# Optimization experiments

Measured on AMD Instinct MI355X. Metric: run time of the kernel, lower is better.

Reference implementation:

```python
import jax, jax.numpy as jnp
import numpy as np

N_NODES = 50000
N_EDGES = 600000
D_IN = 128
D_HID = 256
D_EMB = 128
D_OUT = 2


def sage_conv(x, src, dst, Wl, Wr, b):
    # PyG SAGEConv (aggr='mean'): out_i = W_l @ mean_{j in N(i)} x_j + b + W_r @ x_i
    # edge_index[0]=src (j, message source), edge_index[1]=dst (i, target)
    agg = jax.ops.segment_sum(x[src], dst, num_segments=N_NODES)          # [N, d_in]
    cnt = jax.ops.segment_sum(jnp.ones_like(dst, dtype=x.dtype), dst,
                              num_segments=N_NODES)                        # [N]
    mean = agg / jnp.maximum(cnt, 1.0)[:, None]
    return mean @ Wl + x @ Wr + b


def setup_inputs() -> dict:
    key = jax.random.key(0)
    ks = jax.random.split(key, 12)
    def glorot(k, i, o):
        s = jnp.sqrt(2.0 / (i + o)).astype(jnp.float32)
        return jax.random.normal(k, (i, o), dtype=jnp.float32) * s
    x = jax.random.normal(ks[0], (N_NODES, D_IN), dtype=jnp.float32)
    edge_index = jax.random.randint(ks[1], (2, N_EDGES), 0, N_NODES, dtype=jnp.int64)
    return {
        "x": x,
        "edge_index": edge_index,
        "Wl1": glorot(ks[2], D_IN, D_HID),  "Wr1": glorot(ks[3], D_IN, D_HID),
        "b1": jnp.zeros((D_HID,), jnp.float32),
        "Wl2": glorot(ks[4], D_HID, D_HID), "Wr2": glorot(ks[5], D_HID, D_HID),
        "b2": jnp.zeros((D_HID,), jnp.float32),
        "Wl3": glorot(ks[6], D_HID, D_EMB), "Wr3": glorot(ks[7], D_HID, D_EMB),
        "b3": jnp.zeros((D_EMB,), jnp.float32),
        "Wout": glorot(ks[8], D_EMB, D_OUT),
        "bout": jnp.zeros((D_OUT,), jnp.float32),
    }


def reference(x, edge_index, Wl1, Wr1, b1, Wl2, Wr2, b2, Wl3, Wr3, b3, Wout, bout):
    src, dst = edge_index[0], edge_index[1]
    h = jax.nn.relu(sage_conv(x, src, dst, Wl1, Wr1, b1))   # dropout_rate=0 -> identity
    h = jax.nn.relu(sage_conv(h, src, dst, Wl2, Wr2, b2))
    h = sage_conv(h, src, dst, Wl3, Wr3, b3)
    return h @ Wout + bout                                   # [N, D_OUT]
```

## Files before the change

### kernel.cpp

```cpp
#include <hip/hip_runtime.h>
#include <hip/hip_fp8.h>


constexpr int D_IN  = 128;
constexpr int D_HID = 256;

typedef __attribute__((ext_vector_type(8))) short short8x;
typedef __attribute__((ext_vector_type(4))) float f32x4;
typedef __attribute__((ext_vector_type(2))) float f32x2;

__device__ inline unsigned bf16_rne(float f) {
    unsigned u = __float_as_uint(f);
    return (u + 0x7fffu + ((u >> 16) & 1u)) >> 16;
}


__device__ inline void prep_wt_elem(const float* __restrict__ Wl,
                                    const float* __restrict__ Wr,
                                    int K1, int K2, int Nc, int i,
                                    short* __restrict__ WTh) {
    const int KE = K1 + K2;
    const int KSTEPS = KE / 32;
    int e = i & 7;
    int t = i >> 3;
    int l = t & 63;
    int t2 = t >> 6;
    int k32 = t2 % KSTEPS;
    int n16 = t2 / KSTEPS;
    int n = n16 * 16 + (l & 15);
    int k = k32 * 32 + (l >> 4) * 8 + e;
    float w = (k < K1) ? Wl[(size_t)k * Nc + n] : Wr[(size_t)(k - K1) * Nc + n];
    WTh[i] = (short)bf16_rne(w);
}

__global__ __launch_bounds__(256) void setup_kernel(
    const float* __restrict__ Wl1, const float* __restrict__ Wr1,
    short* __restrict__ wt1h,
    const float* __restrict__ Wl2, const float* __restrict__ Wr2,
    short* __restrict__ wt2h,
    const float* __restrict__ Wl3, const float* __restrict__ Wr3,
    const float* __restrict__ b3, const float* __restrict__ Wout,
    const float* __restrict__ bout, float* __restrict__ Wc, float* __restrict__ bc,
    const float* __restrict__ x, unsigned short* __restrict__ xb,
    const int* __restrict__ dst, int* __restrict__ cnt,
    int Nn, int E) {
    const int gtid = blockIdx.x * blockDim.x + threadIdx.x;
    const int gs = gridDim.x * blockDim.x;

    const int n8 = Nn * D_IN / 8;
    for (int i = gtid; i < n8; i += gs) {
        const float4* p = (const float4*)(x + (size_t)i * 8);
        float4 v0 = p[0], v1 = p[1];
        float f[8] = {v0.x, v0.y, v0.z, v0.w, v1.x, v1.y, v1.z, v1.w};
        unsigned h[8];
        #pragma unroll
        for (int j = 0; j < 8; ++j) h[j] = bf16_rne(f[j]);
        uint4 qh;
        qh.x = h[0] | (h[1] << 16); qh.y = h[2] | (h[3] << 16);
        qh.z = h[4] | (h[5] << 16); qh.w = h[6] | (h[7] << 16);
        *(uint4*)(xb + (size_t)i * 8) = qh;
    }

    for (int i = gtid; i < E; i += gs)
        atomicAdd(&cnt[dst[i]], 1);

    for (int i = gtid; i < 256 * 256; i += gs)
        prep_wt_elem(Wl1, Wr1, 128, 128, 256, i, wt1h);
    for (int i = gtid; i < 256 * 512; i += gs)
        prep_wt_elem(Wl2, Wr2, 256, 256, 256, i, wt2h);

    if (gtid < 1024 * 16) {
        int d = gtid >> 4, sl = gtid & 15;
        int hh = d >> 2, c = d & 3;
        const float* Ws = (c < 2) ? Wl3 : Wr3;
        int o = c & 1;
        float s = 0.f;
        #pragma unroll
        for (int e = 0; e < 8; ++e) {
            int k = sl * 8 + e;
            s += Ws[hh * 128 + k] * Wout[k * 2 + o];
        }
        #pragma unroll
        for (int mk = 8; mk >= 1; mk >>= 1) s += __shfl_xor(s, mk, 16);
        if (sl == 0) Wc[d] = s;
    }
    if (gtid >= 16384 && gtid < 16416) {
        int o = (gtid >> 4) & 1, sl = gtid & 15;
        float s = 0.f;
        #pragma unroll
        for (int e = 0; e < 8; ++e) {
            int k = sl * 8 + e;
            s += b3[k] * Wout[k * 2 + o];
        }
        #pragma unroll
        for (int mk = 8; mk >= 1; mk >>= 1) s += __shfl_xor(s, mk, 16);
        if (sl == 0) bc[o] = s + bout[o];
    }
}


__global__ __launch_bounds__(1024) void scan_local_kernel(
    const int* __restrict__ cnt, int* __restrict__ row_ptr,
    int* __restrict__ bsums, int Nn) {
    __shared__ int wsum[16];
    const int tid = threadIdx.x, lane = tid & 63, wid = tid >> 6;
    const int idx0 = blockIdx.x * 4096 + tid * 4;
    int v[4];
    #pragma unroll
    for (int j = 0; j < 4; ++j) {
        int idx = idx0 + j;
        v[j] = (idx < Nn) ? cnt[idx] : 0;
    }
    int s = v[0] + v[1] + v[2] + v[3];
    int xi = s;
    #pragma unroll
    for (int o = 1; o < 64; o <<= 1) {
        int t = __shfl_up(xi, o, 64);
        if (lane >= o) xi += t;
    }
    if (lane == 63) wsum[wid] = xi;
    __syncthreads();
    if (wid == 0) {
        int t = (lane < 16) ? wsum[lane] : 0;
        #pragma unroll
        for (int o = 1; o < 16; o <<= 1) {
            int u = __shfl_up(t, o, 64);
            if (lane >= o) t += u;
        }
        if (lane < 16) wsum[lane] = t;
    }
    __syncthreads();
    int off = (wid ? wsum[wid - 1] : 0) + xi - s;
    int run = off;
    #pragma unroll
    for (int j = 0; j < 4; ++j) {
        int idx = idx0 + j;
        if (idx <= Nn) row_ptr[idx] = run;
        run += v[j];
    }
    if (tid == 0) bsums[blockIdx.x] = wsum[15];
}

__global__ __launch_bounds__(1024) void scan_add_kernel(
    int* __restrict__ row_ptr, int* __restrict__ cursor,
    const int* __restrict__ bsums, int Nn) {
    __shared__ int sbase;
    const int b = blockIdx.x;
    if (threadIdx.x == 0) {
        int s = 0;
        for (int i = 0; i < b; ++i) s += bsums[i];
        sbase = s;
    }
    __syncthreads();
    const int base = sbase;
    const int idx0 = b * 4096 + threadIdx.x * 4;
    #pragma unroll
    for (int j = 0; j < 4; ++j) {
        int idx = idx0 + j;
        if (idx <= Nn) {
            int v = row_ptr[idx] + base;
            row_ptr[idx] = v;
            if (idx < Nn) cursor[idx] = v;
        }
    }
}

__global__ __launch_bounds__(256) void scatter_kernel(
    const int* __restrict__ src, const int* __restrict__ dst,
    int* __restrict__ cursor, int* __restrict__ esrc, int E) {
    int i0 = (blockIdx.x * blockDim.x + threadIdx.x) * 4;
    if (i0 >= E) return;
    int n = E - i0; if (n > 4) n = 4;
    int s[4], p[4];
    for (int j = 0; j < n; ++j) s[j] = src[i0 + j];
    for (int j = 0; j < n; ++j) p[j] = atomicAdd(&cursor[dst[i0 + j]], 1);
    for (int j = 0; j < n; ++j) esrc[p[j]] = s[j];
}


__device__ inline void addbf8(const uint4& q, float* a) {
    a[0] += __uint_as_float(q.x << 16); a[1] += __uint_as_float(q.x & 0xFFFF0000u);
    a[2] += __uint_as_float(q.y << 16); a[3] += __uint_as_float(q.y & 0xFFFF0000u);
    a[4] += __uint_as_float(q.z << 16); a[5] += __uint_as_float(q.z & 0xFFFF0000u);
    a[6] += __uint_as_float(q.w << 16); a[7] += __uint_as_float(q.w & 0xFFFF0000u);
}

__device__ inline void addf8w(unsigned u, float* a) {
    f32x2 lo = __builtin_amdgcn_cvt_pk_f32_fp8((int)u, false);
    f32x2 hi = __builtin_amdgcn_cvt_pk_f32_fp8((int)u, true);
    a[0] += lo.x; a[1] += lo.y; a[2] += hi.x; a[3] += hi.y;
}

__device__ inline void addf8x16(const uint4& q, float* a) {
    addf8w(q.x, a + 0); addf8w(q.y, a + 4); addf8w(q.z, a + 8); addf8w(q.w, a + 12);
}


template <int K1, int K2, int N, bool RELU, bool TU, bool F8G, bool F8OUT>
__global__ __launch_bounds__(256, 4) void fused_gemm_kernel(
    const void* __restrict__ gsrc, const unsigned short* __restrict__ self,
    const int* __restrict__ row_ptr, const int* __restrict__ esrc,
    const short8x* __restrict__ WTh, const float* __restrict__ bias,
    unsigned short* __restrict__ C, unsigned char* __restrict__ C8,
    const float* __restrict__ Wc, const float* __restrict__ bc,
    float* __restrict__ tuout, int M) {
    constexpr int KEFF = K1 + K2;
    constexpr int KS32 = KEFF / 32;
    constexpr int NC1 = K1 / 8;
    constexpr int NC2 = K2 / 8;
    __shared__ __attribute__((aligned(16))) unsigned short sA[32][KEFF];
    __shared__ float4 sRed[4][32];
    const int tid = threadIdx.x, lane = tid & 63, wid = tid >> 6;
    const int bm = blockIdx.x * 32;

    #pragma unroll
    for (int pass = 0; pass < 2; ++pass) {
        const int nl = pass * 16 + wid * 4 + (lane >> 4);
        const int node = bm + nl;
        const int sl = lane & 15;
        if constexpr (!F8G) {
            float a0[8] = {}, a1[8] = {}, a2[8] = {}, a3[8] = {};
            float inv = 1.0f;
            if (node < M) {
                int beg = row_ptr[node], end = row_ptr[node + 1];
                const unsigned short* xg = (const unsigned short*)gsrc;
                int e = beg;
                for (; e + 4 <= end; e += 4) {
                    int s0 = esrc[e], s1 = esrc[e + 1], s2 = esrc[e + 2], s3 = esrc[e + 3];
                    uint4 q0 = *(const uint4*)(xg + (size_t)s0 * K1 + sl * 8);
                    uint4 q1 = *(const uint4*)(xg + (size_t)s1 * K1 + sl * 8);
                    uint4 q2 = *(const uint4*)(xg + (size_t)s2 * K1 + sl * 8);
                    uint4 q3 = *(const uint4*)(xg + (size_t)s3 * K1 + sl * 8);
                    addbf8(q0, a0); addbf8(q1, a1); addbf8(q2, a2); addbf8(q3, a3);
                }
                for (; e < end; ++e) {
                    uint4 q0 = *(const uint4*)(xg + (size_t)esrc[e] * K1 + sl * 8);
                    addbf8(q0, a0);
                }
                inv = 1.0f / fmaxf((float)(end - beg), 1.0f);
            }
            unsigned h[8];
            #pragma unroll
            for (int i = 0; i < 8; ++i)
                h[i] = bf16_rne((a0[i] + a1[i] + a2[i] + a3[i]) * inv);
            uint4 qh;
            qh.x = h[0] | (h[1] << 16); qh.y = h[2] | (h[3] << 16);
            qh.z = h[4] | (h[5] << 16); qh.w = h[6] | (h[7] << 16);
            int p = (sl & 8) | ((sl & 7) ^ (nl & 7));
            *(uint4*)&sA[nl][p * 8] = qh;
        } else {
            float a0[16] = {}, a1[16] = {};
            float inv = 1.0f;
            if (node < M) {
                int beg = row_ptr[node], end = row_ptr[node + 1];
                const unsigned char* xg = (const unsigned char*)gsrc;
                int e = beg;
                for (; e + 4 <= end; e += 4) {
                    int s0 = esrc[e], s1 = esrc[e + 1], s2 = esrc[e + 2], s3 = esrc[e + 3];
                    uint4 q0 = *(const uint4*)(xg + (size_t)s0 * K1 + sl * 16);
                    uint4 q1 = *(const uint4*)(xg + (size_t)s1 * K1 + sl * 16);
                    uint4 q2 = *(const uint4*)(xg + (size_t)s2 * K1 + sl * 16);
                    uint4 q3 = *(const uint4*)(xg + (size_t)s3 * K1 + sl * 16);
                    addf8x16(q0, a0); addf8x16(q1, a1); addf8x16(q2, a0); addf8x16(q3, a1);
                }
                for (; e < end; ++e) {
                    uint4 q0 = *(const uint4*)(xg + (size_t)esrc[e] * K1 + sl * 16);
                    addf8x16(q0, a0);
                }
                inv = 1.0f / fmaxf((float)(end - beg), 1.0f);
            }
            unsigned h[16];
            #pragma unroll
            for (int i = 0; i < 16; ++i)
                h[i] = bf16_rne((a0[i] + a1[i]) * inv);
            uint4 qa, qb;
            qa.x = h[0]  | (h[1]  << 16); qa.y = h[2]  | (h[3]  << 16);
            qa.z = h[4]  | (h[5]  << 16); qa.w = h[6]  | (h[7]  << 16);
            qb.x = h[8]  | (h[9]  << 16); qb.y = h[10] | (h[11] << 16);
            qb.z = h[12] | (h[13] << 16); qb.w = h[14] | (h[15] << 16);
            int c0 = sl * 2, c1 = sl * 2 + 1;
            int p0 = (c0 & ~7) | ((c0 & 7) ^ (nl & 7));
            int p1 = (c1 & ~7) | ((c1 & 7) ^ (nl & 7));
            *(uint4*)&sA[nl][p0 * 8] = qa;
            *(uint4*)&sA[nl][p1 * 8] = qb;
        }
    }

    {
        const int row = tid >> 3, sub = tid & 7;
        int grow = bm + row; if (grow >= M) grow = M - 1;
        #pragma unroll
        for (int i = 0; i < NC2 / 8; ++i) {
            int cg = sub + 8 * i;
            uint4 v = *(const uint4*)(self + (size_t)grow * K2 + cg * 8);
            int c = NC1 + cg;
            int p = (c & ~7) | ((c & 7) ^ (row & 7));
            *(uint4*)&sA[row][p * 8] = v;
        }
    }
    __syncthreads();

    auto loadB = [&](int ks, short8x* bh) {
        #pragma unroll
        for (int n = 0; n < 4; ++n)
            bh[n] = WTh[((size_t)(wid * 4 + n) * KS32 + ks) * 64 + lane];
    };

    f32x4 acc[2][4];
    #pragma unroll
    for (int m = 0; m < 2; ++m)
        #pragma unroll
        for (int n = 0; n < 4; ++n)
            acc[m][n] = (f32x4){0.f, 0.f, 0.f, 0.f};

    short8x bhC[4], bhN[4];
    loadB(0, bhC);

    #pragma unroll
    for (int ks = 0; ks < KS32; ++ks) {
        if (ks + 1 < KS32) loadB(ks + 1, bhN);
        short8x a[2];
        #pragma unroll
        for (int m = 0; m < 2; ++m) {
            const int row = m * 16 + (lane & 15);
            const int c = ks * 4 + (lane >> 4);
            const int p = (c & ~7) | ((c & 7) ^ (lane & 7));
            a[m] = *(const short8x*)&sA[row][p * 8];
        }
        #pragma unroll
        for (int m = 0; m < 2; ++m)
            #pragma unroll
            for (int n = 0; n < 4; ++n)
                acc[m][n] = __builtin_amdgcn_mfma_f32_16x16x32_bf16(a[m], bhC[n], acc[m][n], 0, 0, 0);
        if (ks + 1 < KS32) {
            #pragma unroll
            for (int n = 0; n < 4; ++n) bhC[n] = bhN[n];
        }
    }

    float bv[4];
    #pragma unroll
    for (int n = 0; n < 4; ++n) bv[n] = bias[wid * 64 + n * 16 + (lane & 15)];

    if constexpr (!TU) {
        #pragma unroll
        for (int n = 0; n < 4; ++n) {
            const int col = wid * 64 + n * 16 + (lane & 15);
            #pragma unroll
            for (int m = 0; m < 2; ++m) {
                #pragma unroll
                for (int j = 0; j < 4; ++j) {
                    int row = bm + m * 16 + (lane >> 4) * 4 + j;
                    if (row < M) {
                        float v = acc[m][n][j] + bv[n];
                        if (RELU) v = fmaxf(v, 0.f);
                        C[(size_t)row * N + col] = (unsigned short)bf16_rne(v);
                        if (F8OUT) {
                            int pk = __builtin_amdgcn_cvt_pk_fp8_f32(v, v, 0, false);
                            C8[(size_t)row * N + col] = (unsigned char)(pk & 0xff);
                        }
                    }
                }
            }
        }
    } else {
        float4 wcv[4];
        #pragma unroll
        for (int n = 0; n < 4; ++n)
            wcv[n] = *(const float4*)(Wc + (size_t)(wid * 64 + n * 16 + (lane & 15)) * 4);
        #pragma unroll
        for (int m = 0; m < 2; ++m) {
            #pragma unroll
            for (int j = 0; j < 4; ++j) {
                float4 p = make_float4(0.f, 0.f, 0.f, 0.f);
                #pragma unroll
                for (int n = 0; n < 4; ++n) {
                    float v = acc[m][n][j] + bv[n];
                    if (RELU) v = fmaxf(v, 0.f);
                    p.x += v * wcv[n].x; p.y += v * wcv[n].y;
                    p.z += v * wcv[n].z; p.w += v * wcv[n].w;
                }
                #pragma unroll
                for (int mk = 8; mk >= 1; mk >>= 1) {
                    p.x += __shfl_xor(p.x, mk, 64);
                    p.y += __shfl_xor(p.y, mk, 64);
                    p.z += __shfl_xor(p.z, mk, 64);
                    p.w += __shfl_xor(p.w, mk, 64);
                }
                if ((lane & 15) == 0)
                    sRed[wid][m * 16 + (lane >> 4) * 4 + j] = p;
            }
        }
        __syncthreads();
        if (tid < 32) {
            int row = bm + tid;
            float4 a = sRed[0][tid], b2 = sRed[1][tid], c2 = sRed[2][tid], d2 = sRed[3][tid];
            float4 t;
            t.x = a.x + b2.x + c2.x + d2.x;
            t.y = a.y + b2.y + c2.y + d2.y;
            t.z = a.z + b2.z + c2.z + d2.z + bc[0];
            t.w = a.w + b2.w + c2.w + d2.w + bc[1];
            if (row < M) *(float4*)(tuout + (size_t)row * 4) = t;
        }
    }
}


__global__ __launch_bounds__(256) void final_out_kernel(
    const float* __restrict__ tu, const int* __restrict__ row_ptr,
    const int* __restrict__ esrc, float* __restrict__ out, int Nn) {
    int stride = gridDim.x * blockDim.x;
    for (int i = blockIdx.x * blockDim.x + threadIdx.x; i < Nn; i += stride) {
        int beg = row_ptr[i], end = row_ptr[i + 1];
        float s0 = 0.f, s1 = 0.f;
        for (int e = beg; e < end; ++e) {
            int s = esrc[e];
            float2 tv = *(const float2*)(tu + (size_t)s * 4);
            s0 += tv.x; s1 += tv.y;
        }
        float inv = 1.0f / fmaxf((float)(end - beg), 1.0f);
        float u0 = tu[(size_t)i * 4 + 2], u1 = tu[(size_t)i * 4 + 3];
        *(float2*)(out + (size_t)i * 2) = make_float2(s0 * inv + u0, s1 * inv + u1);
    }
}


extern "C" void kernel_launch(void* const* d_in, const int* in_sizes, int n_in,
                              void* d_out, int out_size, void* d_ws, size_t ws_size,
                              hipStream_t stream) {
    const float* x    = (const float*)d_in[0];
    const int*   ei   = (const int*)d_in[1];
    const float* Wl1  = (const float*)d_in[2];
    const float* Wr1  = (const float*)d_in[3];
    const float* b1   = (const float*)d_in[4];
    const float* Wl2  = (const float*)d_in[5];
    const float* Wr2  = (const float*)d_in[6];
    const float* b2   = (const float*)d_in[7];
    const float* Wl3  = (const float*)d_in[8];
    const float* Wr3  = (const float*)d_in[9];
    const float* b3   = (const float*)d_in[10];
    const float* Wout = (const float*)d_in[11];
    const float* bout = (const float*)d_in[12];

    const int Nn = in_sizes[0] / D_IN;
    const int E  = in_sizes[1] / 2;

    char* ws = (char*)d_ws;
    size_t off = 0;
    auto alloc = [&](size_t b) { size_t o = off; off = (off + b + 255) & ~(size_t)255; return o; };

    unsigned short* xb    = (unsigned short*)(ws + alloc((size_t)Nn * D_IN * 2));
    int*   row_ptr = (int*)(ws + alloc((size_t)(Nn + 1) * 4));
    int*   cnt     = (int*)(ws + alloc((size_t)Nn * 4));
    int*   cursor  = (int*)(ws + alloc((size_t)Nn * 4));
    int*   bsums   = (int*)(ws + alloc((size_t)256 * 4));
    int*   esrc    = (int*)(ws + alloc((size_t)E * 4));
    unsigned short* h1b   = (unsigned short*)(ws + alloc((size_t)Nn * D_HID * 2));
    unsigned char*  h1f8  = (unsigned char*)(ws + alloc((size_t)Nn * D_HID));
    float* tu      = (float*)(ws + alloc((size_t)Nn * 4 * 4));
    float* Wc      = (float*)(ws + alloc((size_t)256 * 4 * 4));
    float* bc      = (float*)(ws + alloc((size_t)2 * 4));
    short* wt1h    = (short*)(ws + alloc((size_t)256 * 256 * 2));
    short* wt2h    = (short*)(ws + alloc((size_t)256 * 512 * 2));

    const int* src = ei;
    const int* dst = ei + E;

    hipMemsetAsync(cnt, 0, (size_t)Nn * 4, stream);

    setup_kernel<<<2048, 256, 0, stream>>>(
        Wl1, Wr1, wt1h, Wl2, Wr2, wt2h,
        Wl3, Wr3, b3, Wout, bout, Wc, bc,
        x, xb, dst, cnt, Nn, E);

    const int nb = (Nn + 1 + 4095) / 4096;
    scan_local_kernel<<<nb, 1024, 0, stream>>>(cnt, row_ptr, bsums, Nn);
    scan_add_kernel<<<nb, 1024, 0, stream>>>(row_ptr, cursor, bsums, Nn);
    scatter_kernel<<<(E / 4 + 255) / 256, 256, 0, stream>>>(src, dst, cursor, esrc, E);

    const int gm32 = (Nn + 31) / 32;

    fused_gemm_kernel<128, 128, 256, true, false, false, true>
        <<<gm32, 256, 0, stream>>>(xb, xb, row_ptr, esrc,
                                   (const short8x*)wt1h, b1, h1b, h1f8,
                                   nullptr, nullptr, nullptr, Nn);

    fused_gemm_kernel<256, 256, 256, true, true, true, false>
        <<<gm32, 256, 0, stream>>>(h1f8, h1b, row_ptr, esrc,
                                   (const short8x*)wt2h, b2, nullptr, nullptr,
                                   Wc, bc, tu, Nn);

    final_out_kernel<<<512, 256, 0, stream>>>(tu, row_ptr, esrc, (float*)d_out, Nn);
}
```

Before: 192.6 us.

## Record edge rank during degree count to drop scatter atomics; reuse LDS for reduction

The degree-count pass now stores each edge's atomicAdd return value as its rank within its destination. The CSR scatter then computes the position as row_ptr[dst] + rank, with no second round of atomics and no cursor array. This removes 600K contended atomics, at the cost of writing and reading an extra E-sized rank array. The fused GEMM kernel also aliases its reduction buffer onto the sA shared tile, with an added barrier, to cut LDS use.

```diff
diff --git a/kernel.cpp b/kernel.cpp
--- a/kernel.cpp
+++ b/kernel.cpp
@@ -42,7 +42,7 @@
     const float* __restrict__ b3, const float* __restrict__ Wout,
     const float* __restrict__ bout, float* __restrict__ Wc, float* __restrict__ bc,
     const float* __restrict__ x, unsigned short* __restrict__ xb,
-    const int* __restrict__ dst, int* __restrict__ cnt,
+    const int* __restrict__ dst, int* __restrict__ cnt, int* __restrict__ erank,
     int Nn, int E) {
     const int gtid = blockIdx.x * blockDim.x + threadIdx.x;
     const int gs = gridDim.x * blockDim.x;
@@ -62,7 +62,7 @@
     }
 
     for (int i = gtid; i < E; i += gs)
-        atomicAdd(&cnt[dst[i]], 1);
+        erank[i] = atomicAdd(&cnt[dst[i]], 1);
 
     for (int i = gtid; i < 256 * 256; i += gs)
         prep_wt_elem(Wl1, Wr1, 128, 128, 256, i, wt1h);
@@ -142,8 +142,7 @@
 }
 
 __global__ __launch_bounds__(1024) void scan_add_kernel(
-    int* __restrict__ row_ptr, int* __restrict__ cursor,
-    const int* __restrict__ bsums, int Nn) {
+    int* __restrict__ row_ptr, const int* __restrict__ bsums, int Nn) {
     __shared__ int sbase;
     const int b = blockIdx.x;
     if (threadIdx.x == 0) {
@@ -157,24 +156,21 @@
     #pragma unroll
     for (int j = 0; j < 4; ++j) {
         int idx = idx0 + j;
-        if (idx <= Nn) {
-            int v = row_ptr[idx] + base;
-            row_ptr[idx] = v;
-            if (idx < Nn) cursor[idx] = v;
-        }
+        if (idx <= Nn) row_ptr[idx] += base;
     }
 }
 
 __global__ __launch_bounds__(256) void scatter_kernel(
     const int* __restrict__ src, const int* __restrict__ dst,
-    int* __restrict__ cursor, int* __restrict__ esrc, int E) {
+    const int* __restrict__ row_ptr, const int* __restrict__ erank,
+    int* __restrict__ esrc, int E) {
     int i0 = (blockIdx.x * blockDim.x + threadIdx.x) * 4;
     if (i0 >= E) return;
     int n = E - i0; if (n > 4) n = 4;
-    int s[4], p[4];
-    for (int j = 0; j < n; ++j) s[j] = src[i0 + j];
-    for (int j = 0; j < n; ++j) p[j] = atomicAdd(&cursor[dst[i0 + j]], 1);
-    for (int j = 0; j < n; ++j) esrc[p[j]] = s[j];
+    int s[4], d[4], r[4], b[4];
+    for (int j = 0; j < n; ++j) { s[j] = src[i0 + j]; d[j] = dst[i0 + j]; r[j] = erank[i0 + j]; }
+    for (int j = 0; j < n; ++j) b[j] = row_ptr[d[j]];
+    for (int j = 0; j < n; ++j) esrc[b[j] + r[j]] = s[j];
 }
 
 
@@ -209,7 +205,7 @@
     constexpr int NC1 = K1 / 8;
     constexpr int NC2 = K2 / 8;
     __shared__ __attribute__((aligned(16))) unsigned short sA[32][KEFF];
-    __shared__ float4 sRed[4][32];
+    float4* sRed = (float4*)&sA[0][0];
     const int tid = threadIdx.x, lane = tid & 63, wid = tid >> 6;
     const int bm = blockIdx.x * 32;
 
@@ -368,6 +364,7 @@
         #pragma unroll
         for (int n = 0; n < 4; ++n)
             wcv[n] = *(const float4*)(Wc + (size_t)(wid * 64 + n * 16 + (lane & 15)) * 4);
+        __syncthreads();
         #pragma unroll
         for (int m = 0; m < 2; ++m) {
             #pragma unroll
@@ -388,13 +385,14 @@
                     p.w += __shfl_xor(p.w, mk, 64);
                 }
                 if ((lane & 15) == 0)
-                    sRed[wid][m * 16 + (lane >> 4) * 4 + j] = p;
+                    sRed[wid * 32 + m * 16 + (lane >> 4) * 4 + j] = p;
             }
         }
         __syncthreads();
         if (tid < 32) {
             int row = bm + tid;
-            float4 a = sRed[0][tid], b2 = sRed[1][tid], c2 = sRed[2][tid], d2 = sRed[3][tid];
+            float4 a = sRed[0 * 32 + tid], b2 = sRed[1 * 32 + tid];
+            float4 c2 = sRed[2 * 32 + tid], d2 = sRed[3 * 32 + tid];
             float4 t;
             t.x = a.x + b2.x + c2.x + d2.x;
             t.y = a.y + b2.y + c2.y + d2.y;
@@ -452,7 +450,7 @@
     unsigned short* xb    = (unsigned short*)(ws + alloc((size_t)Nn * D_IN * 2));
     int*   row_ptr = (int*)(ws + alloc((size_t)(Nn + 1) * 4));
     int*   cnt     = (int*)(ws + alloc((size_t)Nn * 4));
-    int*   cursor  = (int*)(ws + alloc((size_t)Nn * 4));
+    int*   erank   = (int*)(ws + alloc((size_t)E * 4));
     int*   bsums   = (int*)(ws + alloc((size_t)256 * 4));
     int*   esrc    = (int*)(ws + alloc((size_t)E * 4));
     unsigned short* h1b   = (unsigned short*)(ws + alloc((size_t)Nn * D_HID * 2));
@@ -471,12 +469,12 @@
     setup_kernel<<<2048, 256, 0, stream>>>(
         Wl1, Wr1, wt1h, Wl2, Wr2, wt2h,
         Wl3, Wr3, b3, Wout, bout, Wc, bc,
-        x, xb, dst, cnt, Nn, E);
+        x, xb, dst, cnt, erank, Nn, E);
 
     const int nb = (Nn + 1 + 4095) / 4096;
     scan_local_kernel<<<nb, 1024, 0, stream>>>(cnt, row_ptr, bsums, Nn);
-    scan_add_kernel<<<nb, 1024, 0, stream>>>(row_ptr, cursor, bsums, Nn);
-    scatter_kernel<<<(E / 4 + 255) / 256, 256, 0, stream>>>(src, dst, cursor, esrc, E);
+    scan_add_kernel<<<nb, 1024, 0, stream>>>(row_ptr, bsums, Nn);
+    scatter_kernel<<<(E / 4 + 255) / 256, 256, 0, stream>>>(src, dst, row_ptr, erank, esrc, E);
 
     const int gm32 = (Nn + 31) / 32;
 
```

Result: faster. 180.8 us (-6.2%).
